# Kernel optimization log

Hardware: AMD Instinct MI355X
Metric: run time of the kernel (lower is better)

The kernel has to match this reference:

```python
import jax, jax.numpy as jnp
import numpy as np

D_MODEL = 1024
NUM_HEADS = 16
D_FF = 4096
B, T = 2, 2048
EPS = 1e-5


def setup_inputs() -> dict:
    key = jax.random.key(0)
    ks = jax.random.split(key, 8)
    s = 0.02
    return {
        "x": jax.random.normal(ks[0], (B, T, D_MODEL), dtype=jnp.float32),
        "wq": jax.random.normal(ks[1], (D_MODEL, D_MODEL), dtype=jnp.float32) * s,
        "wk": jax.random.normal(ks[2], (D_MODEL, D_MODEL), dtype=jnp.float32) * s,
        "wv": jax.random.normal(ks[3], (D_MODEL, D_MODEL), dtype=jnp.float32) * s,
        "wo": jax.random.normal(ks[4], (D_MODEL, D_MODEL), dtype=jnp.float32) * s,
        "w1": jax.random.normal(ks[5], (D_FF, D_MODEL), dtype=jnp.float32) * s,
        "w2": jax.random.normal(ks[6], (D_MODEL, D_FF), dtype=jnp.float32) * s,
        "g1": jnp.ones((D_MODEL,), dtype=jnp.float32),
        "g2": jnp.ones((D_MODEL,), dtype=jnp.float32),
    }


def rmsnorm(x, g):
    rms = jnp.sqrt(jnp.mean(x * x, axis=-1, keepdims=True) + EPS)
    return x / rms * g


def gelu(x):
    # exact erf-based GELU, as in the original module
    return 0.5 * x * (1.0 + jax.scipy.special.erf(x / jnp.sqrt(jnp.float32(2.0))))


def attention(x, wq, wk, wv, wo):
    b, t, d = x.shape
    d_k = d // NUM_HEADS
    # torch Linear: y = x @ W.T
    q = (x @ wq.T).reshape(b, t, NUM_HEADS, d_k).transpose(0, 2, 1, 3)
    k = (x @ wk.T).reshape(b, t, NUM_HEADS, d_k).transpose(0, 2, 1, 3)
    v = (x @ wv.T).reshape(b, t, NUM_HEADS, d_k).transpose(0, 2, 1, 3)
    scores = jnp.einsum("bhqd,bhkd->bhqk", q, k) / jnp.sqrt(jnp.float32(d_k))
    causal = jnp.triu(jnp.ones((t, t), dtype=bool), k=1)  # True above diagonal -> masked
    scores = jnp.where(causal, -jnp.inf, scores)
    attn = jax.nn.softmax(scores, axis=-1)
    out = jnp.einsum("bhqk,bhkd->bhqd", attn, v)
    out = out.transpose(0, 2, 1, 3).reshape(b, t, d)
    return out @ wo.T


def reference(x, wq, wk, wv, wo, w1, w2, g1, g2):
    x = x + attention(rmsnorm(x, g1), wq, wk, wv, wo)
    h = rmsnorm(x, g2)
    x = x + gelu(h @ w1.T) @ w2.T
    return x
```

## Files before the change

kernel.cpp:

```cpp
#include <hip/hip_runtime.h>
#include <stdint.h>

#define D_MODEL 1024
#define NUM_HEADS 16
#define D_FF 4096
#define BB 2
#define TT 2048
#define NROWS (BB * TT)

typedef __bf16 bf16x8 __attribute__((ext_vector_type(8)));
typedef short s16x8 __attribute__((ext_vector_type(8)));
typedef float f32x4 __attribute__((ext_vector_type(4)));

static __device__ __forceinline__ f32x4 mfma16(s16x8 a, s16x8 b, f32x4 c) {
  return __builtin_amdgcn_mfma_f32_16x16x32_bf16(
      __builtin_bit_cast(bf16x8, a), __builtin_bit_cast(bf16x8, b), c, 0, 0, 0);
}

static __device__ __forceinline__ short f2b(float f) {
  union { float f; uint32_t u; } v; v.f = f;
  return (short)((v.u + 0x7FFFu + ((v.u >> 16) & 1u)) >> 16);
}

typedef __attribute__((address_space(1))) const unsigned int gu32;
typedef __attribute__((address_space(3))) unsigned int lu32;
static __device__ __forceinline__ void gload16(const short* g, short* l) {
  __builtin_amdgcn_global_load_lds((gu32*)g, (lu32*)l, 16, 0, 0);
}

__global__ __launch_bounds__(256) void rmsnorm_kernel(
    const float* __restrict__ x, const float* __restrict__ g, short* __restrict__ out) {
  const int row = blockIdx.x;
  const int tid = threadIdx.x;
  const float4 xv = *(const float4*)(x + (size_t)row * D_MODEL + tid * 4);
  float ss = xv.x * xv.x + xv.y * xv.y + xv.z * xv.z + xv.w * xv.w;
#pragma unroll
  for (int off = 32; off >= 1; off >>= 1) ss += __shfl_down(ss, off);
  __shared__ float part[4];
  if ((tid & 63) == 0) part[tid >> 6] = ss;
  __syncthreads();
  const float tot = part[0] + part[1] + part[2] + part[3];
  const float sc = rsqrtf(tot * (1.0f / D_MODEL) + 1e-5f);
  const float4 gv = *(const float4*)(g + tid * 4);
  short4 o;
  o.x = f2b(xv.x * sc * gv.x);
  o.y = f2b(xv.y * sc * gv.y);
  o.z = f2b(xv.z * sc * gv.z);
  o.w = f2b(xv.w * sc * gv.w);
  *(short4*)(out + (size_t)row * D_MODEL + tid * 4) = o;
}

__global__ __launch_bounds__(256) void cvt_kernel(
    const float* __restrict__ in, short* __restrict__ out, int n) {
  const int i = (blockIdx.x * 256 + threadIdx.x) * 8;
  if (i >= n) return;
  const float4 a = *(const float4*)(in + i);
  const float4 b = *(const float4*)(in + i + 4);
  union { short s[8]; s16x8 v; } u;
  u.s[0] = f2b(a.x); u.s[1] = f2b(a.y); u.s[2] = f2b(a.z); u.s[3] = f2b(a.w);
  u.s[4] = f2b(b.x); u.s[5] = f2b(b.y); u.s[6] = f2b(b.z); u.s[7] = f2b(b.w);
  *(s16x8*)(out + i) = u.v;
}

__global__ __launch_bounds__(256) void cvt4_kernel(
    const float* __restrict__ a, const float* __restrict__ b,
    const float* __restrict__ c, const float* __restrict__ d,
    short* __restrict__ oa, short* __restrict__ ob,
    short* __restrict__ oc, short* __restrict__ od) {
  const int gid = blockIdx.x * 256 + threadIdx.x;
  const int seg = gid >> 17;
  const int off = (gid & 131071) * 8;
  const float* in = seg == 0 ? a : seg == 1 ? b : seg == 2 ? c : d;
  short* out = seg == 0 ? oa : seg == 1 ? ob : seg == 2 ? oc : od;
  const float4 lo = *(const float4*)(in + off);
  const float4 hi = *(const float4*)(in + off + 4);
  union { short s[8]; s16x8 v; } u;
  u.s[0] = f2b(lo.x); u.s[1] = f2b(lo.y); u.s[2] = f2b(lo.z); u.s[3] = f2b(lo.w);
  u.s[4] = f2b(hi.x); u.s[5] = f2b(hi.y); u.s[6] = f2b(hi.z); u.s[7] = f2b(hi.w);
  *(s16x8*)(out + off) = u.v;
}

template <int MFRAG>
__device__ __forceinline__ void gemm_core(
    const short* __restrict__ A, const short* __restrict__ Bw,
    int Ksl, int lda, int ldb, int brow, int bcol,
    short (&As)[2][MFRAG * 32][32], short (&Bs)[2][128][32],
    f32x4 (*acc)[4]) {
  const int tid = threadIdx.x;
  const int lane = tid & 63, wv = tid >> 6;
  const int l15 = lane & 15, lg = lane >> 4;
  const int wr = wv >> 1, wc = wv & 1;

  const int srow = wv * 16 + (lane >> 2);
  const int csrc = (lane & 3) ^ ((lane >> 3) & 3);
  const int crd = (l15 >> 1) & 3;
  const short* Ag[MFRAG / 2];
  const short* Bg[2];
#pragma unroll
  for (int j = 0; j < MFRAG / 2; ++j)
    Ag[j] = A + (size_t)(brow + j * 64 + srow) * lda + csrc * 8;
#pragma unroll
  for (int j = 0; j < 2; ++j)
    Bg[j] = Bw + (size_t)(bcol + j * 64 + srow) * ldb + csrc * 8;

#pragma unroll
  for (int j = 0; j < MFRAG / 2; ++j)
    gload16(Ag[j], &As[0][0][0] + j * 2048 + wv * 512);
#pragma unroll
  for (int j = 0; j < 2; ++j)
    gload16(Bg[j], &Bs[0][0][0] + j * 2048 + wv * 512);

  int cur = 0;
  for (int k0 = 0; k0 < Ksl; k0 += 32) {
    __syncthreads();
    if (k0 + 32 < Ksl) {
      const int nb = cur ^ 1, ko = k0 + 32;
#pragma unroll
      for (int j = 0; j < MFRAG / 2; ++j)
        gload16(Ag[j] + ko, &As[nb][0][0] + j * 2048 + wv * 512);
#pragma unroll
      for (int j = 0; j < 2; ++j)
        gload16(Bg[j] + ko, &Bs[nb][0][0] + j * 2048 + wv * 512);
    }
    s16x8 af[MFRAG], bfr[4];
#pragma unroll
    for (int m = 0; m < MFRAG; ++m)
      af[m] = *(const s16x8*)&As[cur][wr * (MFRAG * 16) + m * 16 + l15][(lg ^ crd) * 8];
#pragma unroll
    for (int n = 0; n < 4; ++n)
      bfr[n] = *(const s16x8*)&Bs[cur][wc * 64 + n * 16 + l15][(lg ^ crd) * 8];
#pragma unroll
    for (int m = 0; m < MFRAG; ++m)
#pragma unroll
      for (int n = 0; n < 4; ++n)
        acc[m][n] = mfma16(af[m], bfr[n], acc[m][n]);
    cur ^= 1;
  }
}

template <int MODE, int MFRAG>
__global__ __launch_bounds__(256) void gemm_bt(
    const short* __restrict__ A, const short* __restrict__ Bw,
    short* __restrict__ outb, float* __restrict__ outf,
    const float* __restrict__ resid, int Ksl, int lda, int N) {
  __shared__ __align__(16) short As[2][MFRAG * 32][32];
  __shared__ __align__(16) short Bs[2][128][32];
  f32x4 acc[MFRAG][4] = {};
  const int brow = blockIdx.y * (MFRAG * 32), bcol = blockIdx.x * 128;
  const int kz = blockIdx.z * Ksl;
  gemm_core<MFRAG>(A + kz, Bw + kz, Ksl, lda, lda, brow, bcol, As, Bs, acc);

  const int tid = threadIdx.x, lane = tid & 63;
  const int wv = tid >> 6, wr = wv >> 1, wc = wv & 1;
  const int l15 = lane & 15, lg = lane >> 4;
#pragma unroll
  for (int m = 0; m < MFRAG; ++m)
#pragma unroll
    for (int n = 0; n < 4; ++n)
#pragma unroll
      for (int r = 0; r < 4; ++r) {
        const int grow = brow + wr * (MFRAG * 16) + m * 16 + lg * 4 + r;
        const int gcol = bcol + wc * 64 + n * 16 + l15;
        const float v = acc[m][n][r];
        const size_t idx = (size_t)grow * N + gcol;
        if (MODE == 0) {
          outb[idx] = f2b(v);
        } else if (MODE == 2) {
          outf[idx] = v + resid[idx];
        } else if (MODE == 3) {
          outb[idx] = f2b(0.5f * v * (1.0f + erff(v * 0.70710678118f)));
        } else {
          unsafeAtomicAdd(&outf[idx], v);
        }
      }
}

__global__ __launch_bounds__(256) void gemm_qkv(
    const short* __restrict__ A, const short* __restrict__ Wq,
    const short* __restrict__ Wk, const short* __restrict__ Wv,
    short* __restrict__ qout, short* __restrict__ kout, short* __restrict__ vtout) {
  __shared__ __align__(16) short As[2][128][32];
  __shared__ __align__(16) short Bs[2][128][32];
  const int sel = blockIdx.x >> 3;
  const int bcol = (blockIdx.x & 7) * 128;
  const int brow = blockIdx.y * 128;
  const short* Bw = sel == 0 ? Wq : sel == 1 ? Wk : Wv;
  f32x4 acc[4][4] = {};
  gemm_core<4>(A, Bw, 1024, 1024, 1024, brow, bcol, As, Bs, acc);

  const int tid = threadIdx.x, lane = tid & 63;
  const int wv = tid >> 6, wr = wv >> 1, wc = wv & 1;
  const int l15 = lane & 15, lg = lane >> 4;
  short* outb = sel == 0 ? qout : kout;
#pragma unroll
  for (int m = 0; m < 4; ++m)
#pragma unroll
    for (int n = 0; n < 4; ++n)
#pragma unroll
      for (int r = 0; r < 4; ++r) {
        const int grow = brow + wr * 64 + m * 16 + lg * 4 + r;
        const int gcol = bcol + wc * 64 + n * 16 + l15;
        float v = acc[m][n][r];
        if (sel == 0) v *= 0.18033688011f;
        const short vb = f2b(v);
        if (sel < 2) {
          outb[(size_t)grow * 1024 + gcol] = vb;
        } else {
          const int bq = grow >> 11, t = grow & 2047;
          const int hh = gcol >> 6, d = gcol & 63;
          vtout[(((size_t)((bq << 4) + hh) << 6) + d) * 2048 + t] = vb;
        }
      }
}

__global__ __launch_bounds__(256) void attn_kernel(
    const short* __restrict__ qb_, const short* __restrict__ kb,
    const short* __restrict__ vt, short* __restrict__ att) {
  const int i = blockIdx.x;
  const int bh = i & 31, bq = bh >> 4, h = bh & 15;
  const int qtb = (i < 256) ? (15 - (i >> 5)) : ((i >> 5) - 8);
  const int qbase = qtb * 128;
  const int tid = threadIdx.x, lane = tid & 63, w = tid >> 6;
  const int l15 = lane & 15, lg = lane >> 4;

  __shared__ __align__(16) short Ks[2][64][64];
  __shared__ __align__(16) short Vs[2][64][64];
  __shared__ __align__(16) short Ps[4][32][64];

  const short* qhead = qb_ + (size_t)bq * 2048 * 1024 + h * 64;
  const short* khead = kb + (size_t)bq * 2048 * 1024 + h * 64;
  const short* vhead = vt + (size_t)bh * 64 * 2048;

  s16x8 aq[2][2];
#pragma unroll
  for (int mq = 0; mq < 2; ++mq) {
    const short* qp = qhead + (size_t)(qbase + mq * 64 + w * 16 + l15) * 1024 + lg * 8;
    aq[mq][0] = *(const s16x8*)(qp);
    aq[mq][1] = *(const s16x8*)(qp + 32);
  }

  f32x4 acc[2][4] = {};
  float mrow[2][4], lrow[2][4];
#pragma unroll
  for (int mq = 0; mq < 2; ++mq)
#pragma unroll
    for (int r = 0; r < 4; ++r) { mrow[mq][r] = -1e30f; lrow[mq][r] = 0.f; }

  const int ssub = lane >> 3;
  const int gch = (lane & 7) ^ ssub;
  const int swz = l15 & 7;

  const int nkt = qbase / 64 + 2;

#define STAGE_KV(buf, k0)                                                     \
  {                                                                           \
    _Pragma("unroll") for (int j = 0; j < 2; ++j) {                           \
      const int row = j * 32 + w * 8 + ssub;                                  \
      gload16(khead + (size_t)((k0) + row) * 1024 + gch * 8,                  \
              &Ks[buf][0][0] + j * 2048 + w * 512);                           \
      gload16(vhead + (size_t)row * 2048 + (k0) + gch * 8,                    \
              &Vs[buf][0][0] + j * 2048 + w * 512);                           \
    }                                                                         \
  }

  STAGE_KV(0, 0);
  int cur = 0;
  for (int kt = 0; kt < nkt; ++kt) {
    const int k0 = kt * 64;
    __syncthreads();
    if (kt + 1 < nkt) STAGE_KV(cur ^ 1, k0 + 64);

    const bool act0 = (k0 <= qbase + w * 16 + 15);

    s16x8 bk[4][2];
#pragma unroll
    for (int c = 0; c < 4; ++c) {
      const int r = c * 16 + l15;
#pragma unroll
      for (int kh = 0; kh < 2; ++kh)
        bk[c][kh] = *(const s16x8*)&Ks[cur][r][((kh * 4 + lg) ^ swz) * 8];
    }

    f32x4 s[2][4] = {};
    __builtin_amdgcn_s_setprio(1);
#pragma unroll
    for (int mq = 0; mq < 2; ++mq) {
      if (mq == 0 && !act0) continue;
#pragma unroll
      for (int c = 0; c < 4; ++c) {
        s[mq][c] = mfma16(aq[mq][0], bk[c][0], s[mq][c]);
        s[mq][c] = mfma16(aq[mq][1], bk[c][1], s[mq][c]);
      }
    }
    __builtin_amdgcn_s_setprio(0);

#pragma unroll
    for (int mq = 0; mq < 2; ++mq) {
      if (mq == 0 && !act0) continue;
      const int rbase = qbase + mq * 64 + w * 16;
      if (k0 + 63 > rbase) {
#pragma unroll
        for (int c = 0; c < 4; ++c) {
          const int kcol = k0 + c * 16 + l15;
#pragma unroll
          for (int r = 0; r < 4; ++r)
            if (kcol > rbase + lg * 4 + r) s[mq][c][r] = -1e30f;
        }
      }
      float mt[4];
#pragma unroll
      for (int r = 0; r < 4; ++r)
        mt[r] = fmaxf(fmaxf(s[mq][0][r], s[mq][1][r]), fmaxf(s[mq][2][r], s[mq][3][r]));
#pragma unroll
      for (int off = 8; off >= 1; off >>= 1)
#pragma unroll
        for (int r = 0; r < 4; ++r) mt[r] = fmaxf(mt[r], __shfl_xor(mt[r], off));
      bool need = false;
#pragma unroll
      for (int r = 0; r < 4; ++r) need = need || (mt[r] > mrow[mq][r] + 8.0f);
      if (__any(need)) {
#pragma unroll
        for (int r = 0; r < 4; ++r) {
          const float mnew = fmaxf(mrow[mq][r], mt[r]);
          const float scl = exp2f(mrow[mq][r] - mnew);
          mrow[mq][r] = mnew;
          lrow[mq][r] *= scl;
#pragma unroll
          for (int df = 0; df < 4; ++df) acc[mq][df][r] *= scl;
        }
      }
#pragma unroll
      for (int c = 0; c < 4; ++c)
#pragma unroll
        for (int r = 0; r < 4; ++r) {
          const float p = exp2f(s[mq][c][r] - mrow[mq][r]);
          lrow[mq][r] += p;
          const int prow = mq * 16 + lg * 4 + r;
          const int ch = c * 2 + (l15 >> 3);
          Ps[w][prow][((ch ^ (prow & 7)) << 3) + (l15 & 7)] = f2b(p);
        }
    }

    s16x8 bv[4][2];
#pragma unroll
    for (int df = 0; df < 4; ++df) {
      const int r = df * 16 + l15;
#pragma unroll
      for (int kh = 0; kh < 2; ++kh)
        bv[df][kh] = *(const s16x8*)&Vs[cur][r][((kh * 4 + lg) ^ swz) * 8];
    }

    __builtin_amdgcn_s_setprio(1);
#pragma unroll
    for (int mq = 0; mq < 2; ++mq) {
      if (mq == 0 && !act0) continue;
#pragma unroll
      for (int kh = 0; kh < 2; ++kh) {
        const s16x8 pa = *(const s16x8*)&Ps[w][mq * 16 + l15][((kh * 4 + lg) ^ swz) * 8];
#pragma unroll
        for (int df = 0; df < 4; ++df)
          acc[mq][df] = mfma16(pa, bv[df][kh], acc[mq][df]);
      }
    }
    __builtin_amdgcn_s_setprio(0);
    cur ^= 1;
  }

#pragma unroll
  for (int mq = 0; mq < 2; ++mq) {
#pragma unroll
    for (int off = 8; off >= 1; off >>= 1)
#pragma unroll
      for (int r = 0; r < 4; ++r) lrow[mq][r] += __shfl_xor(lrow[mq][r], off);
    float inv[4];
#pragma unroll
    for (int r = 0; r < 4; ++r) inv[r] = 1.0f / lrow[mq][r];
#pragma unroll
    for (int df = 0; df < 4; ++df)
#pragma unroll
      for (int r = 0; r < 4; ++r) {
        const int qrow = qbase + mq * 64 + w * 16 + lg * 4 + r;
        const int d = df * 16 + l15;
        att[((size_t)(bq * 2048) + qrow) * 1024 + h * 64 + d] =
            f2b(acc[mq][df][r] * inv[r]);
      }
  }
}

extern "C" void kernel_launch(void* const* d_in, const int* in_sizes, int n_in,
                              void* d_out, int out_size, void* d_ws, size_t ws_size,
                              hipStream_t stream) {
  const float* x  = (const float*)d_in[0];
  const float* wq = (const float*)d_in[1];
  const float* wk = (const float*)d_in[2];
  const float* wv = (const float*)d_in[3];
  const float* wo = (const float*)d_in[4];
  const float* w1 = (const float*)d_in[5];
  const float* w2 = (const float*)d_in[6];
  const float* g1 = (const float*)d_in[7];
  const float* g2 = (const float*)d_in[8];
  float* out = (float*)d_out;

  char* ws = (char*)d_ws;
  const size_t MB = 1u << 20;
  short* wq_b  = (short*)(ws + 0 * MB);
  short* wk_b  = (short*)(ws + 2 * MB);
  short* wv_b  = (short*)(ws + 4 * MB);
  short* wo_b  = (short*)(ws + 6 * MB);
  short* w1_b  = (short*)(ws + 8 * MB);
  short* w2_b  = (short*)(ws + 16 * MB);
  short* xn_b  = (short*)(ws + 24 * MB);
  short* q_b   = (short*)(ws + 32 * MB);
  short* k_b   = (short*)(ws + 40 * MB);
  short* vt_b  = (short*)(ws + 48 * MB);
  short* att_b = (short*)(ws + 56 * MB);
  short* gel_b = (short*)(ws + 32 * MB);

  rmsnorm_kernel<<<NROWS, 256, 0, stream>>>(x, g1, xn_b);
  cvt4_kernel<<<2048, 256, 0, stream>>>(wq, wk, wv, wo, wq_b, wk_b, wv_b, wo_b);
  cvt_kernel<<<2048, 256, 0, stream>>>(w1, w1_b, 1 << 22);
  cvt_kernel<<<2048, 256, 0, stream>>>(w2, w2_b, 1 << 22);
  gemm_qkv<<<dim3(24, 32), 256, 0, stream>>>(xn_b, wq_b, wk_b, wv_b, q_b, k_b, vt_b);
  attn_kernel<<<512, 256, 0, stream>>>(q_b, k_b, vt_b, att_b);
  gemm_bt<2, 2><<<dim3(8, 64), 256, 0, stream>>>(att_b, wo_b, nullptr, out, x, 1024, 1024, 1024);
  rmsnorm_kernel<<<NROWS, 256, 0, stream>>>(out, g2, xn_b);
  gemm_bt<3, 4><<<dim3(32, 32), 256, 0, stream>>>(xn_b, w1_b, gel_b, nullptr, nullptr, 1024, 1024, 4096);
  gemm_bt<4, 4><<<dim3(8, 32, 2), 256, 0, stream>>>(gel_b, w2_b, nullptr, out, nullptr, 2048, 4096, 1024);
}
```

Baseline: 406.2 us.

## Restructure attention to 8 waves per block with transposed score layout

The attention kernel goes from 4 waves each owning 32 query rows to 8 waves each owning 16 rows, with a 2D grid ordered so the longest query tiles launch first. The QK^T MFMA operands are swapped, so each lane holds one query's scores and the row max needs only two cross-lane shuffles instead of four. Probabilities are packed with v_cvt_pk_bf16_f32 and written transposed as 8-byte stores into LDS. Fully masked waves skip the whole tile body. The change trades fewer registers per wave and more waves for extra shuffles when rescaling and normalizing.

Result: faster. 369.6 us (-9.0%).

```diff
diff --git a/kernel.cpp b/kernel.cpp
--- a/kernel.cpp
+++ b/kernel.cpp
@@ -20,6 +20,12 @@
 static __device__ __forceinline__ short f2b(float f) {
   union { float f; uint32_t u; } v; v.f = f;
   return (short)((v.u + 0x7FFFu + ((v.u >> 16) & 1u)) >> 16);
+}
+
+static __device__ __forceinline__ uint32_t pk2b(float a, float b) {
+  uint32_t r;
+  asm("v_cvt_pk_bf16_f32 %0, %1, %2" : "=v"(r) : "v"(a), "v"(b));
+  return r;
 }
 
 typedef __attribute__((address_space(1))) const unsigned int gu32;
@@ -213,178 +219,159 @@
       }
 }
 
-__global__ __launch_bounds__(256) void attn_kernel(
+__global__ __launch_bounds__(512) void attn_kernel(
     const short* __restrict__ qb_, const short* __restrict__ kb,
     const short* __restrict__ vt, short* __restrict__ att) {
-  const int i = blockIdx.x;
-  const int bh = i & 31, bq = bh >> 4, h = bh & 15;
-  const int qtb = (i < 256) ? (15 - (i >> 5)) : ((i >> 5) - 8);
+  const int bh = blockIdx.x, bq = bh >> 4, h = bh & 15;
+  const int qtb = (int)gridDim.y - 1 - (int)blockIdx.y;
   const int qbase = qtb * 128;
   const int tid = threadIdx.x, lane = tid & 63, w = tid >> 6;
   const int l15 = lane & 15, lg = lane >> 4;
 
   __shared__ __align__(16) short Ks[2][64][64];
   __shared__ __align__(16) short Vs[2][64][64];
-  __shared__ __align__(16) short Ps[4][32][64];
+  __shared__ __align__(16) short PsT[8][16][64];
 
   const short* qhead = qb_ + (size_t)bq * 2048 * 1024 + h * 64;
   const short* khead = kb + (size_t)bq * 2048 * 1024 + h * 64;
   const short* vhead = vt + (size_t)bh * 64 * 2048;
 
-  s16x8 aq[2][2];
-#pragma unroll
-  for (int mq = 0; mq < 2; ++mq) {
-    const short* qp = qhead + (size_t)(qbase + mq * 64 + w * 16 + l15) * 1024 + lg * 8;
-    aq[mq][0] = *(const s16x8*)(qp);
-    aq[mq][1] = *(const s16x8*)(qp + 32);
+  const int wqbase = qbase + w * 16;
+  const int qg = wqbase + l15;
+
+  s16x8 aq0, aq1;
+  {
+    const short* qp = qhead + (size_t)qg * 1024 + lg * 8;
+    aq0 = *(const s16x8*)(qp);
+    aq1 = *(const s16x8*)(qp + 32);
   }
 
-  f32x4 acc[2][4] = {};
-  float mrow[2][4], lrow[2][4];
-#pragma unroll
-  for (int mq = 0; mq < 2; ++mq)
-#pragma unroll
-    for (int r = 0; r < 4; ++r) { mrow[mq][r] = -1e30f; lrow[mq][r] = 0.f; }
-
-  const int ssub = lane >> 3;
-  const int gch = (lane & 7) ^ ssub;
+  f32x4 acc[4] = {};
+  float mrow = -1e30f, lrow = 0.f;
+
+  const int srow = lane >> 3;
+  const int gch = (lane & 7) ^ srow;
   const int swz = l15 & 7;
 
   const int nkt = qbase / 64 + 2;
 
-#define STAGE_KV(buf, k0)                                                     \
+#define STAGE_KV8(buf, k0)                                                    \
   {                                                                           \
-    _Pragma("unroll") for (int j = 0; j < 2; ++j) {                           \
-      const int row = j * 32 + w * 8 + ssub;                                  \
-      gload16(khead + (size_t)((k0) + row) * 1024 + gch * 8,                  \
-              &Ks[buf][0][0] + j * 2048 + w * 512);                           \
-      gload16(vhead + (size_t)row * 2048 + (k0) + gch * 8,                    \
-              &Vs[buf][0][0] + j * 2048 + w * 512);                           \
-    }                                                                         \
+    gload16(khead + (size_t)((k0) + w * 8 + srow) * 1024 + gch * 8,           \
+            &Ks[buf][0][0] + w * 512);                                        \
+    gload16(vhead + (size_t)(w * 8 + srow) * 2048 + (k0) + gch * 8,           \
+            &Vs[buf][0][0] + w * 512);                                        \
   }
 
-  STAGE_KV(0, 0);
+  STAGE_KV8(0, 0);
   int cur = 0;
   for (int kt = 0; kt < nkt; ++kt) {
     const int k0 = kt * 64;
     __syncthreads();
-    if (kt + 1 < nkt) STAGE_KV(cur ^ 1, k0 + 64);
-
-    const bool act0 = (k0 <= qbase + w * 16 + 15);
-
-    s16x8 bk[4][2];
-#pragma unroll
-    for (int c = 0; c < 4; ++c) {
-      const int r = c * 16 + l15;
+    if (kt + 1 < nkt) STAGE_KV8(cur ^ 1, k0 + 64);
+
+    const bool act = (k0 <= wqbase + 15);
+    if (act) {
+      s16x8 bk[4][2];
+#pragma unroll
+      for (int c = 0; c < 4; ++c)
+#pragma unroll
+        for (int kh = 0; kh < 2; ++kh)
+          bk[c][kh] = *(const s16x8*)&Ks[cur][c * 16 + l15][((kh * 4 + lg) ^ swz) * 8];
+
+      f32x4 s[4] = {};
+      __builtin_amdgcn_s_setprio(1);
+#pragma unroll
+      for (int c = 0; c < 4; ++c) {
+        s[c] = mfma16(bk[c][0], aq0, s[c]);
+        s[c] = mfma16(bk[c][1], aq1, s[c]);
+      }
+      __builtin_amdgcn_s_setprio(0);
+
+      if (k0 + 63 > wqbase) {
+#pragma unroll
+        for (int c = 0; c < 4; ++c) {
+          const int kgb = k0 + c * 16 + lg * 4;
+#pragma unroll
+          for (int r = 0; r < 4; ++r)
+            if (kgb + r > qg) s[c][r] = -1e30f;
+        }
+      }
+
+      float mt = s[0][0];
+#pragma unroll
+      for (int c = 0; c < 4; ++c)
+#pragma unroll
+        for (int r = 0; r < 4; ++r) mt = fmaxf(mt, s[c][r]);
+      mt = fmaxf(mt, __shfl_xor(mt, 16));
+      mt = fmaxf(mt, __shfl_xor(mt, 32));
+
+      if (__any(mt > mrow + 8.0f)) {
+        const float mnew = fmaxf(mrow, mt);
+        const float scl = exp2f(mrow - mnew);
+        mrow = mnew;
+        lrow *= scl;
+        float sclT[4];
+#pragma unroll
+        for (int r = 0; r < 4; ++r)
+          sclT[r] = __shfl(scl, (lane & 48) + lg * 4 + r);
+#pragma unroll
+        for (int df = 0; df < 4; ++df)
+#pragma unroll
+          for (int r = 0; r < 4; ++r) acc[df][r] *= sclT[r];
+      }
+
+#pragma unroll
+      for (int c = 0; c < 4; ++c) {
+        float p0 = exp2f(s[c][0] - mrow);
+        float p1 = exp2f(s[c][1] - mrow);
+        float p2 = exp2f(s[c][2] - mrow);
+        float p3 = exp2f(s[c][3] - mrow);
+        lrow += (p0 + p1) + (p2 + p3);
+        uint2 pk;
+        pk.x = pk2b(p0, p1);
+        pk.y = pk2b(p2, p3);
+        const int gsl = (c * 2 + (lg >> 1)) ^ swz;
+        *(uint2*)&PsT[w][l15][gsl * 8 + (lg & 1) * 4] = pk;
+      }
+
+      s16x8 bv[4][2], pa[2];
+#pragma unroll
+      for (int df = 0; df < 4; ++df)
+#pragma unroll
+        for (int kh = 0; kh < 2; ++kh)
+          bv[df][kh] = *(const s16x8*)&Vs[cur][df * 16 + l15][((kh * 4 + lg) ^ swz) * 8];
 #pragma unroll
       for (int kh = 0; kh < 2; ++kh)
-        bk[c][kh] = *(const s16x8*)&Ks[cur][r][((kh * 4 + lg) ^ swz) * 8];
+        pa[kh] = *(const s16x8*)&PsT[w][l15][(((kh * 4 + lg) ^ swz)) * 8];
+
+      __builtin_amdgcn_s_setprio(1);
+#pragma unroll
+      for (int kh = 0; kh < 2; ++kh)
+#pragma unroll
+        for (int df = 0; df < 4; ++df)
+          acc[df] = mfma16(pa[kh], bv[df][kh], acc[df]);
+      __builtin_amdgcn_s_setprio(0);
     }
-
-    f32x4 s[2][4] = {};
-    __builtin_amdgcn_s_setprio(1);
-#pragma unroll
-    for (int mq = 0; mq < 2; ++mq) {
-      if (mq == 0 && !act0) continue;
-#pragma unroll
-      for (int c = 0; c < 4; ++c) {
-        s[mq][c] = mfma16(aq[mq][0], bk[c][0], s[mq][c]);
-        s[mq][c] = mfma16(aq[mq][1], bk[c][1], s[mq][c]);
-      }
-    }
-    __builtin_amdgcn_s_setprio(0);
-
-#pragma unroll
-    for (int mq = 0; mq < 2; ++mq) {
-      if (mq == 0 && !act0) continue;
-      const int rbase = qbase + mq * 64 + w * 16;
-      if (k0 + 63 > rbase) {
-#pragma unroll
-        for (int c = 0; c < 4; ++c) {
-          const int kcol = k0 + c * 16 + l15;
-#pragma unroll
-          for (int r = 0; r < 4; ++r)
-            if (kcol > rbase + lg * 4 + r) s[mq][c][r] = -1e30f;
-        }
-      }
-      float mt[4];
-#pragma unroll
-      for (int r = 0; r < 4; ++r)
-        mt[r] = fmaxf(fmaxf(s[mq][0][r], s[mq][1][r]), fmaxf(s[mq][2][r], s[mq][3][r]));
-#pragma unroll
-      for (int off = 8; off >= 1; off >>= 1)
-#pragma unroll
-        for (int r = 0; r < 4; ++r) mt[r] = fmaxf(mt[r], __shfl_xor(mt[r], off));
-      bool need = false;
-#pragma unroll
-      for (int r = 0; r < 4; ++r) need = need || (mt[r] > mrow[mq][r] + 8.0f);
-      if (__any(need)) {
-#pragma unroll
-        for (int r = 0; r < 4; ++r) {
-          const float mnew = fmaxf(mrow[mq][r], mt[r]);
-          const float scl = exp2f(mrow[mq][r] - mnew);
-          mrow[mq][r] = mnew;
-          lrow[mq][r] *= scl;
-#pragma unroll
-          for (int df = 0; df < 4; ++df) acc[mq][df][r] *= scl;
-        }
-      }
-#pragma unroll
-      for (int c = 0; c < 4; ++c)
-#pragma unroll
-        for (int r = 0; r < 4; ++r) {
-          const float p = exp2f(s[mq][c][r] - mrow[mq][r]);
-          lrow[mq][r] += p;
-          const int prow = mq * 16 + lg * 4 + r;
-          const int ch = c * 2 + (l15 >> 3);
-          Ps[w][prow][((ch ^ (prow & 7)) << 3) + (l15 & 7)] = f2b(p);
-        }
-    }
-
-    s16x8 bv[4][2];
-#pragma unroll
-    for (int df = 0; df < 4; ++df) {
-      const int r = df * 16 + l15;
-#pragma unroll
-      for (int kh = 0; kh < 2; ++kh)
-        bv[df][kh] = *(const s16x8*)&Vs[cur][r][((kh * 4 + lg) ^ swz) * 8];
-    }
-
-    __builtin_amdgcn_s_setprio(1);
-#pragma unroll
-    for (int mq = 0; mq < 2; ++mq) {
-      if (mq == 0 && !act0) continue;
-#pragma unroll
-      for (int kh = 0; kh < 2; ++kh) {
-        const s16x8 pa = *(const s16x8*)&Ps[w][mq * 16 + l15][((kh * 4 + lg) ^ swz) * 8];
-#pragma unroll
-        for (int df = 0; df < 4; ++df)
-          acc[mq][df] = mfma16(pa, bv[df][kh], acc[mq][df]);
-      }
-    }
-    __builtin_amdgcn_s_setprio(0);
     cur ^= 1;
   }
 
-#pragma unroll
-  for (int mq = 0; mq < 2; ++mq) {
-#pragma unroll
-    for (int off = 8; off >= 1; off >>= 1)
-#pragma unroll
-      for (int r = 0; r < 4; ++r) lrow[mq][r] += __shfl_xor(lrow[mq][r], off);
-    float inv[4];
-#pragma unroll
-    for (int r = 0; r < 4; ++r) inv[r] = 1.0f / lrow[mq][r];
-#pragma unroll
-    for (int df = 0; df < 4; ++df)
-#pragma unroll
-      for (int r = 0; r < 4; ++r) {
-        const int qrow = qbase + mq * 64 + w * 16 + lg * 4 + r;
-        const int d = df * 16 + l15;
-        att[((size_t)(bq * 2048) + qrow) * 1024 + h * 64 + d] =
-            f2b(acc[mq][df][r] * inv[r]);
-      }
-  }
+  lrow += __shfl_xor(lrow, 16);
+  lrow += __shfl_xor(lrow, 32);
+  const float linv = 1.0f / lrow;
+  float invT[4];
+#pragma unroll
+  for (int r = 0; r < 4; ++r)
+    invT[r] = __shfl(linv, (lane & 48) + lg * 4 + r);
+#pragma unroll
+  for (int df = 0; df < 4; ++df)
+#pragma unroll
+    for (int r = 0; r < 4; ++r) {
+      const int qrow = wqbase + lg * 4 + r;
+      const int d = df * 16 + l15;
+      att[((size_t)(bq * 2048) + qrow) * 1024 + h * 64 + d] =
+          f2b(acc[df][r] * invT[r]);
+    }
 }
 
 extern "C" void kernel_launch(void* const* d_in, const int* in_sizes, int n_in,
@@ -421,7 +408,7 @@
   cvt_kernel<<<2048, 256, 0, stream>>>(w1, w1_b, 1 << 22);
   cvt_kernel<<<2048, 256, 0, stream>>>(w2, w2_b, 1 << 22);
   gemm_qkv<<<dim3(24, 32), 256, 0, stream>>>(xn_b, wq_b, wk_b, wv_b, q_b, k_b, vt_b);
-  attn_kernel<<<512, 256, 0, stream>>>(q_b, k_b, vt_b, att_b);
+  attn_kernel<<<dim3(32, 16), 512, 0, stream>>>(q_b, k_b, vt_b, att_b);
   gemm_bt<2, 2><<<dim3(8, 64), 256, 0, stream>>>(att_b, wo_b, nullptr, out, x, 1024, 1024, 1024);
   rmsnorm_kernel<<<NROWS, 256, 0, stream>>>(out, g2, xn_b);
   gemm_bt<3, 4><<<dim3(32, 32), 256, 0, stream>>>(xn_b, w1_b, gel_b, nullptr, nullptr, 1024, 1024, 4096);
```
